# Optimization experiments

Hardware: AMD Instinct MI355X
Metric: run time of the kernel (lower is better)

Reference implementation:

```python
import jax, jax.numpy as jnp
import numpy as np

NUM_HEADS = 16


def setup_inputs() -> dict:
    key = jax.random.key(0)
    ks = jax.random.split(key, 9)
    B, N, E = 2, 2048, 1024
    s = 1.0 / np.sqrt(E).astype(np.float32)
    inp = {"x": jax.random.normal(ks[0], (B, N, E), jnp.float32)}
    names = ["q", "k", "v", "o"]
    for i, n in enumerate(names):
        inp[f"W{n}"] = jax.random.normal(ks[1 + 2 * i], (E, E), jnp.float32) * s
        inp[f"b{n}"] = jax.random.normal(ks[2 + 2 * i], (E,), jnp.float32) * 0.01
    return inp


def _feature(x):
    # act_fun = '1+elu'
    return jax.nn.elu(x) + 1.0


def reference(x, Wq, bq, Wk, bk, Wv, bv, Wo, bo):
    B, N, E = x.shape
    H = NUM_HEADS
    d = E // H

    def proj(t, W, b):  # torch nn.Linear: t @ W^T + b
        return t @ W.T + b

    def split_heads(t):  # (B,N,E) -> (B,H,N,d)
        return t.reshape(B, N, H, d).transpose(0, 2, 1, 3)

    q = _feature(split_heads(proj(x, Wq, bq)))
    k = _feature(split_heads(proj(x, Wk, bk)))
    v = split_heads(proj(x, Wv, bv))

    # causal linear attention: o_t = q_t @ cumsum_{s<=t} (k_s v_s^T)
    kv = jnp.cumsum(k[..., :, None] * v[..., None, :], axis=2)  # (B,H,N,d,d)
    o = jnp.einsum('bhnd,bhnde->bhne', q, kv)                   # (B,H,N,d)

    o = o.transpose(0, 2, 1, 3).reshape(B, N, E)
    return o @ Wo.T + bo
```

## Files before the change

### kernel.cpp

```cpp
#include <hip/hip_runtime.h>
#include <hip/hip_bf16.h>
#include <cmath>

typedef unsigned short u16;
typedef __bf16 bf16x8 __attribute__((ext_vector_type(8)));
typedef float  f32x4  __attribute__((ext_vector_type(4)));
typedef float  f4     __attribute__((ext_vector_type(4)));
typedef u16    us4    __attribute__((ext_vector_type(4)));

#define DEVFN __device__ __forceinline__

static constexpr int Bq = 2, Nq = 2048, Eq = 1024;
static constexpr int Mq = Bq * Nq;
static constexpr int CHK = 64;
static constexpr int NC  = Nq / CHK;
static constexpr int BH  = Bq * 16;

DEVFN u16 f2b(float f) {
    union { float f; unsigned int u; } x; x.f = f;
    unsigned int r = x.u + 0x7fffu + ((x.u >> 16) & 1u);
    return (u16)(r >> 16);
}
DEVFN float b2f(u16 v) {
    union { unsigned int u; float f; } x; x.u = ((unsigned int)v) << 16; return x.f;
}

DEVFN void gl_lds16(const u16* g, u16* l) {
    __builtin_amdgcn_global_load_lds(
        (const __attribute__((address_space(1))) unsigned int*)(g),
        (__attribute__((address_space(3))) unsigned int*)(l),
        16, 0, 0);
}

__global__ __launch_bounds__(256)
void cvt_all_kernel(const float* __restrict__ x,
                    const float* __restrict__ w0, const float* __restrict__ w1,
                    const float* __restrict__ w2, const float* __restrict__ w3,
                    u16* __restrict__ Xb, u16* __restrict__ Wb)
{
    const int blk = blockIdx.x;
    const float* s; u16* d; int i;
    if (blk < 4096) {
        i = blk * 256 + threadIdx.x;  s = x;  d = Xb;
    } else {
        const int wsel = (blk - 4096) >> 10;
        i = ((blk - 4096) & 1023) * 256 + threadIdx.x;
        s = (wsel == 0) ? w0 : (wsel == 1) ? w1 : (wsel == 2) ? w2 : w3;
        d = Wb + (size_t)wsel * (Eq * Eq);
    }
    f4 v = *reinterpret_cast<const f4*>(&s[(size_t)i * 4]);
    us4 p; p[0] = f2b(v[0]); p[1] = f2b(v[1]); p[2] = f2b(v[2]); p[3] = f2b(v[3]);
    *reinterpret_cast<us4*>(&d[(size_t)i * 4]) = p;
}

template<int MODE>
__global__ __launch_bounds__(256)
void gemm_ring(const u16* __restrict__ X, const u16* __restrict__ W,
               const float* __restrict__ b0, const float* __restrict__ b1,
               const float* __restrict__ b2,
               u16* __restrict__ Qb, u16* __restrict__ Kb, u16* __restrict__ KbT,
               u16* __restrict__ VbT, float* __restrict__ outF)
{
    constexpr int BM  = (MODE == 0) ? 128 : 64;
    constexpr int MI  = BM / 32;
    constexpr int AI  = BM / 64;
    constexpr int BUF = BM * 32 + 4096;
    constexpr int NT  = 32;
    __shared__ u16 lds[3 * BUF];

    const int tid = threadIdx.x, wid = tid >> 6, lane = tid & 63;
    const int fid = (MODE == 0) ? ((blockIdx.x & 7) * 96 + (blockIdx.x >> 3))
                                : ((blockIdx.x & 7) * 64 + (blockIdx.x >> 3));
    const int bx  = (MODE == 0) ? (fid % 24) : (fid & 7);
    const int by  = (MODE == 0) ? (fid / 24) : (fid >> 3);
    const int m0  = by * BM, n0 = bx * 128;
    const int wr  = (wid >> 1) * (BM / 2), wc = (wid & 1) * 64;
    const int fr  = lane & 15, fq = lane >> 4;

    const int srow0 = tid >> 2;
    const int scol  = ((tid & 3) ^ (srow0 & 3)) * 8;
    const u16* gA = X + (size_t)(m0 + srow0) * 1024 + scol;
    const u16* gB = W + (size_t)(n0 + srow0) * 1024 + scol;
    const int dA = wid * 512;
    const int dB = BM * 32 + wid * 512;

    const int fsw = (fq ^ (fr & 3)) << 3;
    int aoff[MI], boff[4];
#pragma unroll
    for (int mi = 0; mi < MI; ++mi) aoff[mi] = (wr + mi * 16 + fr) * 32 + fsw;
#pragma unroll
    for (int ni = 0; ni < 4; ++ni)  boff[ni] = BM * 32 + (wc + ni * 16 + fr) * 32 + fsw;

#define STAGE(kt, bsel) do {                                                   \
        const int _k = (kt) * 32;                                              \
        u16* _b = lds + (bsel) * BUF;                                          \
        _Pragma("unroll")                                                      \
        for (int it = 0; it < AI; ++it)                                        \
            gl_lds16(gA + _k + (size_t)it * 64 * 1024, _b + dA + it * 2048);   \
        _Pragma("unroll")                                                      \
        for (int it = 0; it < 2; ++it)                                         \
            gl_lds16(gB + _k + (size_t)it * 64 * 1024, _b + dB + it * 2048);   \
    } while (0)

    STAGE(0, 0);
    STAGE(1, 1);
    if (MODE == 0) asm volatile("s_waitcnt vmcnt(4)" ::: "memory");
    else           asm volatile("s_waitcnt vmcnt(3)" ::: "memory");
    __builtin_amdgcn_s_barrier();
    __builtin_amdgcn_sched_barrier(0);

    f32x4 acc[MI][4] = {};
    int cb = 0, sb = 2;

    for (int t = 0; t < NT; ++t) {
        if (t + 2 < NT) STAGE(t + 2, sb);
        const u16* buf = lds + cb * BUF;
        bf16x8 af[MI], bfv[4];
#pragma unroll
        for (int mi = 0; mi < MI; ++mi)
            af[mi] = *reinterpret_cast<const bf16x8*>(&buf[aoff[mi]]);
#pragma unroll
        for (int ni = 0; ni < 4; ++ni)
            bfv[ni] = *reinterpret_cast<const bf16x8*>(&buf[boff[ni]]);
#pragma unroll
        for (int mi = 0; mi < MI; ++mi)
#pragma unroll
            for (int ni = 0; ni < 4; ++ni)
                acc[mi][ni] = __builtin_amdgcn_mfma_f32_16x16x32_bf16(
                    af[mi], bfv[ni], acc[mi][ni], 0, 0, 0);
        if (t < NT - 2) {
            if (MODE == 0) asm volatile("s_waitcnt vmcnt(4)" ::: "memory");
            else           asm volatile("s_waitcnt vmcnt(3)" ::: "memory");
        } else if (t == NT - 2) {
            asm volatile("s_waitcnt vmcnt(0)" ::: "memory");
        }
        __builtin_amdgcn_s_barrier();
        __builtin_amdgcn_sched_barrier(0);
        cb = (cb == 2) ? 0 : cb + 1;
        sb = (sb == 2) ? 0 : sb + 1;
    }
#undef STAGE

    if (MODE == 0) {
        const int seg = n0 >> 10;
        const float* bp = (seg == 0) ? b0 : (seg == 1) ? b1 : b2;
#pragma unroll
        for (int mi = 0; mi < MI; ++mi)
#pragma unroll
            for (int ni = 0; ni < 4; ++ni) {
                const int nl    = (n0 & 1023) + wc + ni * 16 + fr;
                const int mbase = m0 + wr + mi * 16 + fq * 4;
                const float bn  = bp[nl];
                float vr[4];
#pragma unroll
                for (int r = 0; r < 4; ++r) {
                    float v = acc[mi][ni][r] + bn;
                    if (seg < 2) v = (v > 0.f) ? (v + 1.f) : __expf(v);
                    vr[r] = v;
                }
                if (seg == 0) {
#pragma unroll
                    for (int r = 0; r < 4; ++r)
                        Qb[(size_t)(mbase + r) * 1024 + nl] = f2b(vr[r]);
                } else {
                    us4 pk;
#pragma unroll
                    for (int r = 0; r < 4; ++r) pk[r] = f2b(vr[r]);
                    const int bb = mbase >> 11, nt = mbase & 2047;
                    const int hh = nl >> 6,     dd = nl & 63;
                    u16* T = (seg == 1) ? KbT : VbT;
                    *reinterpret_cast<us4*>(
                        &T[((size_t)(bb * 16 + hh) * 64 + dd) * 2048 + nt]) = pk;
                    if (seg == 1) {
#pragma unroll
                        for (int r = 0; r < 4; ++r)
                            Kb[(size_t)(mbase + r) * 1024 + nl] = f2b(vr[r]);
                    }
                }
            }
    } else {
#pragma unroll
        for (int mi = 0; mi < MI; ++mi)
#pragma unroll
            for (int ni = 0; ni < 4; ++ni) {
                const int n     = n0 + wc + ni * 16 + fr;
                const int mbase = m0 + wr + mi * 16 + fq * 4;
                const float bn  = b0[n];
#pragma unroll
                for (int r = 0; r < 4; ++r)
                    outF[(size_t)(mbase + r) * 1024 + n] = acc[mi][ni][r] + bn;
            }
    }
}

__global__ __launch_bounds__(64)
void chunk_kv_kernel(const u16* __restrict__ KbT, const u16* __restrict__ VbT,
                     u16* __restrict__ KVT)
{
    const int blk = blockIdx.x;
    const int bh = blk >> 5, c = blk & 31;
    const int lane = threadIdx.x;
    const int fr = lane & 15, fq = lane >> 4, fk = fq * 8;
    const u16* kt = KbT + (size_t)bh * 64 * 2048;
    const u16* vt = VbT + (size_t)bh * 64 * 2048;

    bf16x8 a[4][2], b[4][2];
#pragma unroll
    for (int mi = 0; mi < 4; ++mi)
#pragma unroll
        for (int kh = 0; kh < 2; ++kh)
            a[mi][kh] = *reinterpret_cast<const bf16x8*>(
                &vt[(size_t)(mi * 16 + fr) * 2048 + c * 64 + kh * 32 + fk]);
#pragma unroll
    for (int ni = 0; ni < 4; ++ni)
#pragma unroll
        for (int kh = 0; kh < 2; ++kh)
            b[ni][kh] = *reinterpret_cast<const bf16x8*>(
                &kt[(size_t)(ni * 16 + fr) * 2048 + c * 64 + kh * 32 + fk]);

    f32x4 acc[4][4] = {};
#pragma unroll
    for (int mi = 0; mi < 4; ++mi)
#pragma unroll
        for (int ni = 0; ni < 4; ++ni)
#pragma unroll
            for (int kh = 0; kh < 2; ++kh)
                acc[mi][ni] = __builtin_amdgcn_mfma_f32_16x16x32_bf16(
                    a[mi][kh], b[ni][kh], acc[mi][ni], 0, 0, 0);

    u16* out = KVT + (size_t)blk * 4096;
#pragma unroll
    for (int mi = 0; mi < 4; ++mi)
#pragma unroll
        for (int ni = 0; ni < 4; ++ni)
#pragma unroll
            for (int r = 0; r < 4; ++r)
                out[(mi * 16 + fq * 4 + r) * 64 + ni * 16 + fr] = f2b(acc[mi][ni][r]);
}

__global__ __launch_bounds__(256)
void scan_kernel(const u16* __restrict__ KVT, u16* __restrict__ STb)
{
    const int bh = blockIdx.x >> 4, sl = blockIdx.x & 15;
    const int el = sl * 256 + threadIdx.x;
    const u16* src = KVT + (size_t)bh * NC * 4096 + el;
    u16*      dst  = STb + (size_t)bh * NC * 4096 + el;
    float run = 0.f;
#pragma unroll 4
    for (int c = 0; c < NC; ++c) {
        dst[(size_t)c * 4096] = f2b(run);
        run += b2f(src[(size_t)c * 4096]);
    }
}

__global__ __launch_bounds__(64)
void attn_kernel(const u16* __restrict__ Qb, const u16* __restrict__ Kb,
                 const u16* __restrict__ VbT, const u16* __restrict__ STb,
                 u16* __restrict__ Ob)
{
    __shared__ u16 P[64 * 72];
    const int blk = blockIdx.x;
    const int bh = blk >> 5, c = blk & 31;
    const int b = bh >> 4, h = bh & 15;
    const int lane = threadIdx.x;
    const int fr = lane & 15, fq = lane >> 4, fk = fq * 8;
    const int tok0 = b * 2048 + c * 64;

    bf16x8 qa[4][2];
#pragma unroll
    for (int mi = 0; mi < 4; ++mi)
#pragma unroll
        for (int kh = 0; kh < 2; ++kh)
            qa[mi][kh] = *reinterpret_cast<const bf16x8*>(
                &Qb[(size_t)(tok0 + mi * 16 + fr) * 1024 + h * 64 + kh * 32 + fk]);

    {
        bf16x8 kb[4][2];
#pragma unroll
        for (int si = 0; si < 4; ++si)
#pragma unroll
            for (int kh = 0; kh < 2; ++kh)
                kb[si][kh] = *reinterpret_cast<const bf16x8*>(
                    &Kb[(size_t)(tok0 + si * 16 + fr) * 1024 + h * 64 + kh * 32 + fk]);
        f32x4 p[4][4] = {};
#pragma unroll
        for (int mi = 0; mi < 4; ++mi)
#pragma unroll
            for (int si = 0; si < 4; ++si)
#pragma unroll
                for (int kh = 0; kh < 2; ++kh)
                    p[mi][si] = __builtin_amdgcn_mfma_f32_16x16x32_bf16(
                        qa[mi][kh], kb[si][kh], p[mi][si], 0, 0, 0);
#pragma unroll
        for (int mi = 0; mi < 4; ++mi)
#pragma unroll
            for (int si = 0; si < 4; ++si)
#pragma unroll
                for (int r = 0; r < 4; ++r) {
                    int t = mi * 16 + fq * 4 + r;
                    int s = si * 16 + fr;
                    float v = (s <= t) ? p[mi][si][r] : 0.0f;
                    P[t * 72 + s] = f2b(v);
                }
    }
    __syncthreads();

    f32x4 acc[4][4] = {};
    {
        const u16* st = STb + (size_t)blk * 4096;
        bf16x8 sb[4][2];
#pragma unroll
        for (int ni = 0; ni < 4; ++ni)
#pragma unroll
            for (int kh = 0; kh < 2; ++kh)
                sb[ni][kh] = *reinterpret_cast<const bf16x8*>(
                    &st[(ni * 16 + fr) * 64 + kh * 32 + fk]);
#pragma unroll
        for (int mi = 0; mi < 4; ++mi)
#pragma unroll
            for (int ni = 0; ni < 4; ++ni)
#pragma unroll
                for (int kh = 0; kh < 2; ++kh)
                    acc[mi][ni] = __builtin_amdgcn_mfma_f32_16x16x32_bf16(
                        qa[mi][kh], sb[ni][kh], acc[mi][ni], 0, 0, 0);
    }
    {
        const u16* vt = VbT + (size_t)bh * 64 * 2048;
#pragma unroll
        for (int sh = 0; sh < 2; ++sh) {
            bf16x8 pa[4], vb[4];
#pragma unroll
            for (int mi = 0; mi < 4; ++mi)
                pa[mi] = *reinterpret_cast<const bf16x8*>(
                    &P[(mi * 16 + fr) * 72 + sh * 32 + fk]);
#pragma unroll
            for (int ni = 0; ni < 4; ++ni)
                vb[ni] = *reinterpret_cast<const bf16x8*>(
                    &vt[(size_t)(ni * 16 + fr) * 2048 + c * 64 + sh * 32 + fk]);
#pragma unroll
            for (int mi = 0; mi < 4; ++mi)
#pragma unroll
                for (int ni = 0; ni < 4; ++ni)
                    acc[mi][ni] = __builtin_amdgcn_mfma_f32_16x16x32_bf16(
                        pa[mi], vb[ni], acc[mi][ni], 0, 0, 0);
        }
    }
#pragma unroll
    for (int mi = 0; mi < 4; ++mi)
#pragma unroll
        for (int ni = 0; ni < 4; ++ni)
#pragma unroll
            for (int r = 0; r < 4; ++r) {
                int t = tok0 + mi * 16 + fq * 4 + r;
                int n = h * 64 + ni * 16 + fr;
                Ob[(size_t)t * 1024 + n] = f2b(acc[mi][ni][r]);
            }
}

extern "C" void kernel_launch(void* const* d_in, const int* in_sizes, int n_in,
                              void* d_out, int out_size, void* d_ws, size_t ws_size,
                              hipStream_t stream)
{
    (void)in_sizes; (void)n_in; (void)out_size; (void)ws_size;
    const float* x  = (const float*)d_in[0];
    const float* Wq = (const float*)d_in[1];
    const float* bq = (const float*)d_in[2];
    const float* Wk = (const float*)d_in[3];
    const float* bk = (const float*)d_in[4];
    const float* Wv = (const float*)d_in[5];
    const float* bv = (const float*)d_in[6];
    const float* Wo = (const float*)d_in[7];
    const float* bo = (const float*)d_in[8];
    float* out = (float*)d_out;

    char* ws = (char*)d_ws;
    constexpr size_t SZ_ME = (size_t)Mq * Eq * 2;
    u16*   Qb  = (u16*)  (ws + 0 * SZ_ME);
    u16*   Kb  = (u16*)  (ws + 1 * SZ_ME);
    u16*   KbT = (u16*)  (ws + 2 * SZ_ME);
    u16*   VbT = (u16*)  (ws + 3 * SZ_ME);
    u16*   Ob  = (u16*)  (ws + 4 * SZ_ME);
    u16*   KVT = (u16*)  (ws + 5 * SZ_ME);
    u16*   STb = (u16*)  (ws + 6 * SZ_ME);
    u16*   Xb  = (u16*)  (ws + 7 * SZ_ME);
    u16*   Wb0 = (u16*)  (ws + 8 * SZ_ME);
    u16* Wqkvb = Wb0;
    u16* Wob   = Wb0 + (size_t)3 * Eq * Eq;

    cvt_all_kernel<<<dim3(8192), dim3(256), 0, stream>>>(x, Wq, Wk, Wv, Wo, Xb, Wb0);

    gemm_ring<0><<<dim3(768), dim3(256), 0, stream>>>(
        Xb, Wqkvb, bq, bk, bv, Qb, Kb, KbT, VbT, nullptr);

    chunk_kv_kernel<<<dim3(BH * NC), dim3(64), 0, stream>>>(KbT, VbT, KVT);
    scan_kernel<<<dim3(BH * 16), dim3(256), 0, stream>>>(KVT, STb);
    attn_kernel<<<dim3(BH * NC), dim3(64), 0, stream>>>(Qb, Kb, VbT, STb, Ob);

    gemm_ring<1><<<dim3(512), dim3(256), 0, stream>>>(
        Ob, Wob, bo, nullptr, nullptr, nullptr, nullptr, nullptr, nullptr, out);
}
```

Baseline: 92.23 us.

## Halve GEMM workgroup to two waves with wider per-wave tiles and MFMA priority

The projection GEMMs now run with 128 threads (two waves) per block instead of four. Each wave covers half the block rows and all 128 columns, so it holds twice as many accumulators and reuses each A fragment across eight B fragments. The LDS swizzle changes to match the new load pattern, and the vmcnt waits are adjusted for the extra loads per thread. s_setprio is raised around the MFMA bursts in all compute kernels. The aim is more MFMA work per LDS read and better overlap, at the cost of higher register pressure and fewer waves to hide latency.

```diff
diff --git a/kernel.cpp b/kernel.cpp
--- a/kernel.cpp
+++ b/kernel.cpp
@@ -54,92 +54,96 @@
 }
 
 template<int MODE>
-__global__ __launch_bounds__(256)
+__global__ __launch_bounds__(128, 2)
 void gemm_ring(const u16* __restrict__ X, const u16* __restrict__ W,
                const float* __restrict__ b0, const float* __restrict__ b1,
                const float* __restrict__ b2,
                u16* __restrict__ Qb, u16* __restrict__ Kb, u16* __restrict__ KbT,
                u16* __restrict__ VbT, float* __restrict__ outF)
 {
-    constexpr int BM  = (MODE == 0) ? 128 : 64;
-    constexpr int MI  = BM / 32;
-    constexpr int AI  = BM / 64;
-    constexpr int BUF = BM * 32 + 4096;
-    constexpr int NT  = 32;
-    __shared__ u16 lds[3 * BUF];
+    constexpr int BM   = (MODE == 0) ? 128 : 64;
+    constexpr int MI   = BM / 32;
+    constexpr int AR   = BM / 32;
+    constexpr int BUFU = (BM + 128) * 32;
+    constexpr int NT   = 32;
+    __shared__ u16 lds[3 * BUFU];
 
     const int tid = threadIdx.x, wid = tid >> 6, lane = tid & 63;
-    const int fid = (MODE == 0) ? ((blockIdx.x & 7) * 96 + (blockIdx.x >> 3))
-                                : ((blockIdx.x & 7) * 64 + (blockIdx.x >> 3));
+    const int bid = blockIdx.x;
+    const int fid = (MODE == 0) ? ((bid & 7) * 96 + (bid >> 3))
+                                : ((bid & 7) * 64 + (bid >> 3));
     const int bx  = (MODE == 0) ? (fid % 24) : (fid & 7);
     const int by  = (MODE == 0) ? (fid / 24) : (fid >> 3);
     const int m0  = by * BM, n0 = bx * 128;
-    const int wr  = (wid >> 1) * (BM / 2), wc = (wid & 1) * 64;
+    const int wr  = wid * (BM / 2);
     const int fr  = lane & 15, fq = lane >> 4;
 
-    const int srow0 = tid >> 2;
-    const int scol  = ((tid & 3) ^ (srow0 & 3)) * 8;
-    const u16* gA = X + (size_t)(m0 + srow0) * 1024 + scol;
-    const u16* gB = W + (size_t)(n0 + srow0) * 1024 + scol;
-    const int dA = wid * 512;
-    const int dB = BM * 32 + wid * 512;
-
-    const int fsw = (fq ^ (fr & 3)) << 3;
-    int aoff[MI], boff[4];
+    const int row0 = tid >> 2;
+    const int ssw  = ((tid & 3) ^ ((row0 >> 1) & 3)) * 8;
+    const u16* gA = X + (size_t)(m0 + row0) * 1024 + ssw;
+    const u16* gB = W + (size_t)(n0 + row0) * 1024 + ssw;
+    const int dstA = wid * 512;
+    const int dstB = BM * 32 + wid * 512;
+
+    const int fsw = (fq ^ ((fr >> 1) & 3)) << 3;
+    int aoff[MI], boff[8];
 #pragma unroll
     for (int mi = 0; mi < MI; ++mi) aoff[mi] = (wr + mi * 16 + fr) * 32 + fsw;
 #pragma unroll
-    for (int ni = 0; ni < 4; ++ni)  boff[ni] = BM * 32 + (wc + ni * 16 + fr) * 32 + fsw;
+    for (int ni = 0; ni < 8; ++ni)  boff[ni] = BM * 32 + (ni * 16 + fr) * 32 + fsw;
 
 #define STAGE(kt, bsel) do {                                                   \
         const int _k = (kt) * 32;                                              \
-        u16* _b = lds + (bsel) * BUF;                                          \
+        u16* _b = lds + (bsel) * BUFU;                                         \
         _Pragma("unroll")                                                      \
-        for (int it = 0; it < AI; ++it)                                        \
-            gl_lds16(gA + _k + (size_t)it * 64 * 1024, _b + dA + it * 2048);   \
+        for (int it = 0; it < AR; ++it)                                        \
+            gl_lds16(gA + _k + (size_t)it * 32 * 1024, _b + dstA + it * 1024); \
         _Pragma("unroll")                                                      \
-        for (int it = 0; it < 2; ++it)                                         \
-            gl_lds16(gB + _k + (size_t)it * 64 * 1024, _b + dB + it * 2048);   \
+        for (int it = 0; it < 4; ++it)                                         \
+            gl_lds16(gB + _k + (size_t)it * 32 * 1024, _b + dstB + it * 1024); \
+    } while (0)
+
+#define VM_WAIT_STEADY() do {                                                  \
+        if (MODE == 0) asm volatile("s_waitcnt vmcnt(8)" ::: "memory");        \
+        else           asm volatile("s_waitcnt vmcnt(6)" ::: "memory");        \
     } while (0)
 
     STAGE(0, 0);
     STAGE(1, 1);
-    if (MODE == 0) asm volatile("s_waitcnt vmcnt(4)" ::: "memory");
-    else           asm volatile("s_waitcnt vmcnt(3)" ::: "memory");
+    VM_WAIT_STEADY();
+    __builtin_amdgcn_sched_barrier(0);
     __builtin_amdgcn_s_barrier();
-    __builtin_amdgcn_sched_barrier(0);
-
-    f32x4 acc[MI][4] = {};
+
+    f32x4 acc[MI][8] = {};
     int cb = 0, sb = 2;
 
     for (int t = 0; t < NT; ++t) {
         if (t + 2 < NT) STAGE(t + 2, sb);
-        const u16* buf = lds + cb * BUF;
-        bf16x8 af[MI], bfv[4];
+        const u16* buf = lds + cb * BUFU;
+        bf16x8 af[MI], bfv[8];
 #pragma unroll
         for (int mi = 0; mi < MI; ++mi)
             af[mi] = *reinterpret_cast<const bf16x8*>(&buf[aoff[mi]]);
 #pragma unroll
-        for (int ni = 0; ni < 4; ++ni)
+        for (int ni = 0; ni < 8; ++ni)
             bfv[ni] = *reinterpret_cast<const bf16x8*>(&buf[boff[ni]]);
+        __builtin_amdgcn_s_setprio(1);
 #pragma unroll
         for (int mi = 0; mi < MI; ++mi)
 #pragma unroll
-            for (int ni = 0; ni < 4; ++ni)
+            for (int ni = 0; ni < 8; ++ni)
                 acc[mi][ni] = __builtin_amdgcn_mfma_f32_16x16x32_bf16(
                     af[mi], bfv[ni], acc[mi][ni], 0, 0, 0);
-        if (t < NT - 2) {
-            if (MODE == 0) asm volatile("s_waitcnt vmcnt(4)" ::: "memory");
-            else           asm volatile("s_waitcnt vmcnt(3)" ::: "memory");
-        } else if (t == NT - 2) {
-            asm volatile("s_waitcnt vmcnt(0)" ::: "memory");
-        }
+        __builtin_amdgcn_s_setprio(0);
+        if (t < NT - 2)       VM_WAIT_STEADY();
+        else if (t == NT - 2) asm volatile("s_waitcnt vmcnt(0)" ::: "memory");
+        __builtin_amdgcn_sched_barrier(0);
         __builtin_amdgcn_s_barrier();
-        __builtin_amdgcn_sched_barrier(0);
         cb = (cb == 2) ? 0 : cb + 1;
         sb = (sb == 2) ? 0 : sb + 1;
     }
 #undef STAGE
+#undef VM_WAIT_STEADY
 
     if (MODE == 0) {
         const int seg = n0 >> 10;
@@ -147,8 +151,8 @@
 #pragma unroll
         for (int mi = 0; mi < MI; ++mi)
 #pragma unroll
-            for (int ni = 0; ni < 4; ++ni) {
-                const int nl    = (n0 & 1023) + wc + ni * 16 + fr;
+            for (int ni = 0; ni < 8; ++ni) {
+                const int nl    = (n0 & 1023) + ni * 16 + fr;
                 const int mbase = m0 + wr + mi * 16 + fq * 4;
                 const float bn  = bp[nl];
                 float vr[4];
@@ -182,8 +186,8 @@
 #pragma unroll
         for (int mi = 0; mi < MI; ++mi)
 #pragma unroll
-            for (int ni = 0; ni < 4; ++ni) {
-                const int n     = n0 + wc + ni * 16 + fr;
+            for (int ni = 0; ni < 8; ++ni) {
+                const int n     = n0 + ni * 16 + fr;
                 const int mbase = m0 + wr + mi * 16 + fq * 4;
                 const float bn  = b0[n];
 #pragma unroll
@@ -219,6 +223,7 @@
                 &kt[(size_t)(ni * 16 + fr) * 2048 + c * 64 + kh * 32 + fk]);
 
     f32x4 acc[4][4] = {};
+    __builtin_amdgcn_s_setprio(1);
 #pragma unroll
     for (int mi = 0; mi < 4; ++mi)
 #pragma unroll
@@ -227,6 +232,7 @@
             for (int kh = 0; kh < 2; ++kh)
                 acc[mi][ni] = __builtin_amdgcn_mfma_f32_16x16x32_bf16(
                     a[mi][kh], b[ni][kh], acc[mi][ni], 0, 0, 0);
+    __builtin_amdgcn_s_setprio(0);
 
     u16* out = KVT + (size_t)blk * 4096;
 #pragma unroll
@@ -283,6 +289,7 @@
                 kb[si][kh] = *reinterpret_cast<const bf16x8*>(
                     &Kb[(size_t)(tok0 + si * 16 + fr) * 1024 + h * 64 + kh * 32 + fk]);
         f32x4 p[4][4] = {};
+        __builtin_amdgcn_s_setprio(1);
 #pragma unroll
         for (int mi = 0; mi < 4; ++mi)
 #pragma unroll
@@ -291,6 +298,7 @@
                 for (int kh = 0; kh < 2; ++kh)
                     p[mi][si] = __builtin_amdgcn_mfma_f32_16x16x32_bf16(
                         qa[mi][kh], kb[si][kh], p[mi][si], 0, 0, 0);
+        __builtin_amdgcn_s_setprio(0);
 #pragma unroll
         for (int mi = 0; mi < 4; ++mi)
 #pragma unroll
@@ -315,6 +323,7 @@
             for (int kh = 0; kh < 2; ++kh)
                 sb[ni][kh] = *reinterpret_cast<const bf16x8*>(
                     &st[(ni * 16 + fr) * 64 + kh * 32 + fk]);
+        __builtin_amdgcn_s_setprio(1);
 #pragma unroll
         for (int mi = 0; mi < 4; ++mi)
 #pragma unroll
@@ -323,6 +332,7 @@
                 for (int kh = 0; kh < 2; ++kh)
                     acc[mi][ni] = __builtin_amdgcn_mfma_f32_16x16x32_bf16(
                         qa[mi][kh], sb[ni][kh], acc[mi][ni], 0, 0, 0);
+        __builtin_amdgcn_s_setprio(0);
     }
     {
         const u16* vt = VbT + (size_t)bh * 64 * 2048;
@@ -337,12 +347,14 @@
             for (int ni = 0; ni < 4; ++ni)
                 vb[ni] = *reinterpret_cast<const bf16x8*>(
                     &vt[(size_t)(ni * 16 + fr) * 2048 + c * 64 + sh * 32 + fk]);
+            __builtin_amdgcn_s_setprio(1);
 #pragma unroll
             for (int mi = 0; mi < 4; ++mi)
 #pragma unroll
                 for (int ni = 0; ni < 4; ++ni)
                     acc[mi][ni] = __builtin_amdgcn_mfma_f32_16x16x32_bf16(
                         pa[mi], vb[ni], acc[mi][ni], 0, 0, 0);
+            __builtin_amdgcn_s_setprio(0);
         }
     }
 #pragma unroll
@@ -389,13 +401,13 @@
 
     cvt_all_kernel<<<dim3(8192), dim3(256), 0, stream>>>(x, Wq, Wk, Wv, Wo, Xb, Wb0);
 
-    gemm_ring<0><<<dim3(768), dim3(256), 0, stream>>>(
+    gemm_ring<0><<<dim3(768), dim3(128), 0, stream>>>(
         Xb, Wqkvb, bq, bk, bv, Qb, Kb, KbT, VbT, nullptr);
 
     chunk_kv_kernel<<<dim3(BH * NC), dim3(64), 0, stream>>>(KbT, VbT, KVT);
     scan_kernel<<<dim3(BH * 16), dim3(256), 0, stream>>>(KVT, STb);
     attn_kernel<<<dim3(BH * NC), dim3(64), 0, stream>>>(Qb, Kb, VbT, STb, Ob);
 
-    gemm_ring<1><<<dim3(512), dim3(256), 0, stream>>>(
+    gemm_ring<1><<<dim3(512), dim3(128), 0, stream>>>(
         Ob, Wob, bo, nullptr, nullptr, nullptr, nullptr, nullptr, nullptr, out);
 }
```

Measured after the change: 94.66 us. 1.03x slower.
